# Kernel tuning notes

Hardware: AMD Instinct MI355X
Metric: run time of the kernel (lower is better)

## Reference

```python
import jax, jax.numpy as jnp
import numpy as np

DIM = 512
HEADS = 8
HEAD_DIM = DIM // HEADS


def setup_inputs() -> dict:
    key = jax.random.key(0)
    ks = jax.random.split(key, 9)
    B, T, C = 8, 8192, DIM
    s = 1.0 / np.sqrt(C)
    x = jax.random.normal(ks[0], (B, T, C), dtype=jnp.float32)
    Wq = jax.random.uniform(ks[1], (C, C), jnp.float32, -s, s)
    bq = jax.random.uniform(ks[2], (C,), jnp.float32, -s, s)
    Wk = jax.random.uniform(ks[3], (C, C), jnp.float32, -s, s)
    bk = jax.random.uniform(ks[4], (C,), jnp.float32, -s, s)
    Wv = jax.random.uniform(ks[5], (C, C), jnp.float32, -s, s)
    bv = jax.random.uniform(ks[6], (C,), jnp.float32, -s, s)
    Wo = jax.random.uniform(ks[7], (C, C), jnp.float32, -s, s)
    bo = jax.random.uniform(ks[8], (C,), jnp.float32, -s, s)
    return {"x": x, "Wq": Wq, "bq": bq, "Wk": Wk, "bk": bk,
            "Wv": Wv, "bv": bv, "Wo": Wo, "bo": bo}


def reference(x, Wq, bq, Wk, bk, Wv, bv, Wo, bo):
    B, T, C = x.shape
    H, D = HEADS, HEAD_DIM
    # projections -> [B, H, T, D]
    def proj(W, b):
        return (x @ W.T + b).reshape(B, T, H, D).transpose(0, 2, 1, 3)
    Q = proj(Wq, bq)
    K = proj(Wk, bk)
    V = proj(Wv, bv)
    # ELU+1 feature map
    Q = jax.nn.elu(Q) + 1.0
    K = jax.nn.elu(K) + 1.0
    # running KV sum (non-causal global sum) and normalizer
    KV = jnp.einsum('bhnd,bhne->bhde', K, V)          # [B,H,D,D]
    Q_KV = jnp.einsum('bhnd,bhde->bhne', Q, KV)       # [B,H,T,D]
    K_sum = K.sum(axis=2)                              # [B,H,D]
    normalizer = jnp.einsum('bhnd,bhd->bhn', Q, K_sum)  # [B,H,T]
    out = Q_KV / (normalizer[..., None] + 1e-6)
    out = out.transpose(0, 2, 1, 3).reshape(B, T, C)
    out = out @ Wo.T + bo  # dropout is identity in eval mode
    return out
```

## Files before the change

### kernel.cpp

```cpp
#include <hip/hip_runtime.h>
#include <hip/hip_bf16.h>


typedef unsigned short u16t;
typedef unsigned int   u32t;
typedef __bf16 v8bf __attribute__((ext_vector_type(8)));
typedef u16t   v8u  __attribute__((ext_vector_type(8)));
typedef float  v4f  __attribute__((ext_vector_type(4)));

static __device__ __forceinline__ float bf2f(u16t b) {
    u32t u = ((u32t)b) << 16;
    return __builtin_bit_cast(float, u);
}
static __device__ __forceinline__ u16t f2bf(float f) {
    u32t u = __builtin_bit_cast(u32t, f);
    u += 0x7fffu + ((u >> 16) & 1u);
    return (u16t)(u >> 16);
}
static __device__ __forceinline__ v8u cvt8(const float* p) {
    const float4 a = *(const float4*)p;
    const float4 b = *(const float4*)(p + 4);
    v8u r;
    r[0] = f2bf(a.x); r[1] = f2bf(a.y); r[2] = f2bf(a.z); r[3] = f2bf(a.w);
    r[4] = f2bf(b.x); r[5] = f2bf(b.y); r[6] = f2bf(b.z); r[7] = f2bf(b.w);
    return r;
}

#define GLDS16(g, l) __builtin_amdgcn_global_load_lds(                       \
        (const __attribute__((address_space(1))) void*)(g),                  \
        (__attribute__((address_space(3))) void*)(l), 16, 0, 0)

__global__ __launch_bounds__(256) void cvt_x(
        const float* __restrict__ src, u16t* __restrict__ dst) {
    const int i = (blockIdx.x * 256 + threadIdx.x) * 8;
    *(v8u*)&dst[i] = cvt8(&src[i]);
}

__global__ __launch_bounds__(256) void cvt_wb(
        const float* __restrict__ Wq, const float* __restrict__ Wk,
        const float* __restrict__ Wv, const float* __restrict__ Wo,
        const float* __restrict__ bq, const float* __restrict__ bk,
        const float* __restrict__ bv, const float* __restrict__ bo,
        u16t* __restrict__ Wpack, u16t* __restrict__ bpack) {
    const int b = blockIdx.x;
    if (b < 512) {
        const int gidx = (b * 256 + threadIdx.x) * 8;
        const int seg = gidx >> 18;
        const int off = gidx & 262143;
        const float* src = (seg == 0) ? Wq : (seg == 1) ? Wk
                          : (seg == 2) ? Wv : Wo;
        *(v8u*)&Wpack[gidx] = cvt8(&src[off]);
    } else {
        const int seg = b - 512;
        const float* src = (seg == 0) ? bq : (seg == 1) ? bk
                          : (seg == 2) ? bv : bo;
        if (threadIdx.x < 64) {
            const int off = threadIdx.x * 8;
            *(v8u*)&bpack[seg * 512 + off] = cvt8(&src[off]);
        }
    }
}

static __device__ __forceinline__ void gemm_core(
        const u16t* __restrict__ A, const u16t* __restrict__ W,
        size_t mbase, int nbase, u16t* sm, v4f acc[4][4], int tid) {
    const int w    = tid >> 6;
    const int lane = tid & 63;
    const int quad = lane >> 4;
    const int l16  = lane & 15;
    const int wm   = (w & 1) * 64;
    const int wn   = (w >> 1) * 64;

#pragma unroll
    for (int i = 0; i < 4; ++i)
#pragma unroll
        for (int j = 0; j < 4; ++j) acc[i][j] = (v4f){0.f, 0.f, 0.f, 0.f};

    const int r0 = w * 32 + (lane >> 2);
    const int r1 = r0 + 16;
    const int cs = ((lane & 3) ^ ((lane >> 3) & 3)) * 8;
    const u16t* pa0 = A + (mbase + r0) * 512 + cs;
    const u16t* pa1 = A + (mbase + r1) * 512 + cs;
    const u16t* pb0 = W + (size_t)(nbase + r0) * 512 + cs;
    const u16t* pb1 = W + (size_t)(nbase + r1) * 512 + cs;
    u16t* const la = sm + w * 1024 + lane * 8;
    u16t* const lb = sm + 8192 + w * 1024 + lane * 8;

#define GC_ISSUE(buf)                                                        \
    do {                                                                     \
        GLDS16(pa0, la + (buf) * 4096);                                      \
        GLDS16(pa1, la + (buf) * 4096 + 512);                                \
        GLDS16(pb0, lb + (buf) * 4096);                                      \
        GLDS16(pb1, lb + (buf) * 4096 + 512);                                \
        pa0 += 32; pa1 += 32; pb0 += 32; pb1 += 32;                          \
    } while (0)

    GC_ISSUE(0);
    __syncthreads();

    const int sA = (quad ^ ((l16 >> 1) & 3)) * 8;
    int cur = 0;
#pragma unroll
    for (int kt = 0; kt < 16; ++kt) {
        if (kt < 15) GC_ISSUE(cur ^ 1);
        const u16t* Ab = sm + cur * 4096;
        const u16t* Bb = sm + 8192 + cur * 4096;
        v8bf af[4], bfr[4];
#pragma unroll
        for (int mi = 0; mi < 4; ++mi)
            af[mi] = *(const v8bf*)&Ab[(wm + mi * 16 + l16) * 32 + sA];
#pragma unroll
        for (int ni = 0; ni < 4; ++ni)
            bfr[ni] = *(const v8bf*)&Bb[(wn + ni * 16 + l16) * 32 + sA];
#pragma unroll
        for (int mi = 0; mi < 4; ++mi)
#pragma unroll
            for (int ni = 0; ni < 4; ++ni)
                acc[mi][ni] = __builtin_amdgcn_mfma_f32_16x16x32_bf16(
                    af[mi], bfr[ni], acc[mi][ni], 0, 0, 0);
        __syncthreads();
        cur ^= 1;
    }
#undef GC_ISSUE
}

__global__ __launch_bounds__(256) void qkv_gemm(
        const u16t* __restrict__ xb, const u16t* __restrict__ Wpack,
        const u16t* __restrict__ bpack,
        u16t* __restrict__ Qb, u16t* __restrict__ Kb, u16t* __restrict__ Vb) {
    __shared__ __align__(16) u16t sm[16384];
    const u32t id = blockIdx.x;
    const u32t wg = (id & 7) * 768 + (id >> 3);
    const int sub = (int)(wg % 12u);
    const int p = sub >> 2;
    const int nbase = (sub & 3) * 128;
    const size_t mbase = (size_t)(wg / 12u) * 128;
    const u16t* W = Wpack + (size_t)p * 262144;
    const u16t* bias = bpack + p * 512;
    u16t* C = (p == 0) ? Qb : (p == 1) ? Kb : Vb;
    const bool elu = (p < 2);
    const int tid = threadIdx.x;
    const int w = tid >> 6, lane = tid & 63, quad = lane >> 4, l16 = lane & 15;
    const int wn = (w >> 1) * 64;

    v4f acc[4][4];
    gemm_core(xb, W, mbase, nbase, sm, acc, tid);

    u16t (*Cs)[132] = (u16t(*)[132])sm;
#pragma unroll
    for (int pass = 0; pass < 2; ++pass) {
        if ((w & 1) == pass) {
#pragma unroll
            for (int ni = 0; ni < 4; ++ni) {
                const int lcol = wn + ni * 16 + l16;
                const float bb = bf2f(bias[nbase + lcol]);
#pragma unroll
                for (int mi = 0; mi < 4; ++mi)
#pragma unroll
                    for (int r = 0; r < 4; ++r) {
                        float v = acc[mi][ni][r] + bb;
                        if (elu) v = (v > 0.f) ? (v + 1.f) : __expf(v);
                        Cs[mi * 16 + quad * 4 + r][lcol] = f2bf(v);
                    }
            }
        }
        __syncthreads();
#pragma unroll
        for (int rep = 0; rep < 4; ++rep) {
            const int f = rep * 256 + tid;
            const int row = f >> 4;
            const int c8 = (f & 15) * 8;
            const uint2 lo = *(const uint2*)&Cs[row][c8];
            const uint2 hi = *(const uint2*)&Cs[row][c8 + 4];
            const uint4 val = make_uint4(lo.x, lo.y, hi.x, hi.y);
            *(uint4*)&C[(mbase + pass * 64 + row) * 512 + nbase + c8] = val;
        }
        __syncthreads();
    }
}

__global__ __launch_bounds__(256) void out_gemm(
        const u16t* __restrict__ attn, const u16t* __restrict__ Wo,
        const u16t* __restrict__ bo, float* __restrict__ C) {
    __shared__ __align__(16) u16t sm[16384];
    const u32t id = blockIdx.x;
    const u32t wg = (id & 7) * 256 + (id >> 3);
    const int nbase = (int)(wg & 3u) * 128;
    const size_t mbase = (size_t)(wg >> 2) * 128;
    const int tid = threadIdx.x;
    const int w = tid >> 6, lane = tid & 63, quad = lane >> 4, l16 = lane & 15;
    const int wn = (w >> 1) * 64;

    v4f acc[4][4];
    gemm_core(attn, Wo, mbase, nbase, sm, acc, tid);

    float (*Cf)[132] = (float(*)[132])sm;
#pragma unroll
    for (int p = 0; p < 4; ++p) {
        if ((w & 1) == (p >> 1)) {
#pragma unroll
            for (int ni = 0; ni < 4; ++ni) {
                const int lcol = wn + ni * 16 + l16;
                const float bb = bf2f(bo[nbase + lcol]);
#pragma unroll
                for (int m2 = 0; m2 < 2; ++m2) {
                    const int mi = (p & 1) * 2 + m2;
#pragma unroll
                    for (int r = 0; r < 4; ++r)
                        Cf[m2 * 16 + quad * 4 + r][lcol] = acc[mi][ni][r] + bb;
                }
            }
        }
        __syncthreads();
#pragma unroll
        for (int rep = 0; rep < 4; ++rep) {
            const int f = rep * 256 + tid;
            const int row = f >> 5;
            const int c4 = (f & 31) * 4;
            *(float4*)&C[(mbase + p * 32 + row) * 512 + nbase + c4] =
                *(const float4*)&Cf[row][c4];
        }
        __syncthreads();
    }
}

__global__ __launch_bounds__(256) void kv_reduce(
        const u16t* __restrict__ Kp, const u16t* __restrict__ Vp,
        float* __restrict__ Part) {
    __shared__ u16t Kl[64][66];
    __shared__ u16t Vl[64][66];
    const u32t id  = blockIdx.x;
    const u32t swz = (id & 7) * 128 + (id >> 3);
    const int h     = (int)(swz & 7);
    const int grp   = (int)(swz >> 3);
    const int b     = grp >> 4;
    const int chunk = grp & 15;
    const int bh    = b * 8 + h;
    const int tid = threadIdx.x;
    const int w = tid >> 6, lane = tid & 63, quad = lane >> 4, l16 = lane & 15;
    const int trow0 = tid >> 3;
    const int c8 = (tid & 7) * 8;

    v4f acc[4];
#pragma unroll
    for (int i = 0; i < 4; ++i) acc[i] = (v4f){0.f, 0.f, 0.f, 0.f};
    float ks[8];
#pragma unroll
    for (int j = 0; j < 8; ++j) ks[j] = 0.f;

    size_t g0 = ((size_t)b * 8192 + chunk * 512 + trow0) * 512 + h * 64 + c8;
    size_t g1 = g0 + 32 * 512;
    uint4 kq0 = *(const uint4*)&Kp[g0];
    uint4 kq1 = *(const uint4*)&Kp[g1];
    uint4 vq0 = *(const uint4*)&Vp[g0];
    uint4 vq1 = *(const uint4*)&Vp[g1];

    for (int tile = 0; tile < 8; ++tile) {
        *(u32t*)&Kl[trow0][c8 + 0] = kq0.x;
        *(u32t*)&Kl[trow0][c8 + 2] = kq0.y;
        *(u32t*)&Kl[trow0][c8 + 4] = kq0.z;
        *(u32t*)&Kl[trow0][c8 + 6] = kq0.w;
        *(u32t*)&Kl[trow0 + 32][c8 + 0] = kq1.x;
        *(u32t*)&Kl[trow0 + 32][c8 + 2] = kq1.y;
        *(u32t*)&Kl[trow0 + 32][c8 + 4] = kq1.z;
        *(u32t*)&Kl[trow0 + 32][c8 + 6] = kq1.w;
        *(u32t*)&Vl[trow0][c8 + 0] = vq0.x;
        *(u32t*)&Vl[trow0][c8 + 2] = vq0.y;
        *(u32t*)&Vl[trow0][c8 + 4] = vq0.z;
        *(u32t*)&Vl[trow0][c8 + 6] = vq0.w;
        *(u32t*)&Vl[trow0 + 32][c8 + 0] = vq1.x;
        *(u32t*)&Vl[trow0 + 32][c8 + 2] = vq1.y;
        *(u32t*)&Vl[trow0 + 32][c8 + 4] = vq1.z;
        *(u32t*)&Vl[trow0 + 32][c8 + 6] = vq1.w;
        {
            const v8u ku0 = __builtin_bit_cast(v8u, kq0);
            const v8u ku1 = __builtin_bit_cast(v8u, kq1);
#pragma unroll
            for (int j = 0; j < 8; ++j)
                ks[j] += bf2f(ku0[j]) + bf2f(ku1[j]);
        }
        __syncthreads();
        if (tile < 7) {
            g0 += 64 * 512; g1 += 64 * 512;
            kq0 = *(const uint4*)&Kp[g0];
            kq1 = *(const uint4*)&Kp[g1];
            vq0 = *(const uint4*)&Vp[g0];
            vq1 = *(const uint4*)&Vp[g1];
        }
#pragma unroll
        for (int ts = 0; ts < 2; ++ts) {
            v8u au;
#pragma unroll
            for (int j = 0; j < 8; ++j)
                au[j] = Kl[ts * 32 + quad * 8 + j][w * 16 + l16];
            const v8bf af = __builtin_bit_cast(v8bf, au);
#pragma unroll
            for (int et = 0; et < 4; ++et) {
                v8u bu;
#pragma unroll
                for (int j = 0; j < 8; ++j)
                    bu[j] = Vl[ts * 32 + quad * 8 + j][et * 16 + l16];
                acc[et] = __builtin_amdgcn_mfma_f32_16x16x32_bf16(
                    af, __builtin_bit_cast(v8bf, bu), acc[et], 0, 0, 0);
            }
        }
        __syncthreads();
    }

    const size_t pbase = (size_t)(bh * 16 + chunk) * 4160;
#pragma unroll
    for (int et = 0; et < 4; ++et)
#pragma unroll
        for (int r = 0; r < 4; ++r)
            Part[pbase + (size_t)(w * 16 + quad * 4 + r) * 64 + et * 16 + l16]
                = acc[et][r];

    float* kr = (float*)&Kl[0][0];
#pragma unroll
    for (int j = 0; j < 8; ++j) kr[trow0 * 65 + c8 + j] = ks[j];
    __syncthreads();
    if (tid < 64) {
        float s = 0.f;
#pragma unroll
        for (int g = 0; g < 32; ++g) s += kr[g * 65 + tid];
        Part[pbase + 4096 + tid] = s;
    }
}

__global__ __launch_bounds__(256) void kv_pack(
        const float* __restrict__ Part, u16t* __restrict__ KVb,
        float* __restrict__ Ks) {
    __shared__ float kvs[64][64];
    const int bh = blockIdx.x;
    const int tid = threadIdx.x;
    const size_t base = (size_t)bh * 16 * 4160;
#pragma unroll
    for (int rr = 0; rr < 4; ++rr) {
        const int fi = rr * 256 + tid;
        const int d = fi >> 4;
        const int e4 = (fi & 15) * 4;
        float4 s = make_float4(0.f, 0.f, 0.f, 0.f);
        for (int c = 0; c < 16; ++c) {
            const float4 p =
                *(const float4*)&Part[base + (size_t)c * 4160 + d * 64 + e4];
            s.x += p.x; s.y += p.y; s.z += p.z; s.w += p.w;
        }
        *(float4*)&kvs[d][e4] = s;
    }
    if (tid < 64) {
        float s = 0.f;
        for (int c = 0; c < 16; ++c)
            s += Part[base + (size_t)c * 4160 + 4096 + tid];
        Ks[bh * 64 + tid] = s;
    }
    __syncthreads();
#pragma unroll
    for (int i = 0; i < 2; ++i) {
        const int c = tid + i * 256;
        const int ksi = c >> 8;
        const int nb = (c >> 6) & 3;
        const int L = c & 63;
        const int quad = L >> 4, l16 = L & 15;
        v8u pk;
#pragma unroll
        for (int j = 0; j < 8; ++j)
            pk[j] = f2bf(kvs[ksi * 32 + quad * 8 + j][nb * 16 + l16]);
        *(v8u*)&KVb[((size_t)bh * 512 + c) * 8] = pk;
    }
}

__global__ __launch_bounds__(256) void attn_apply(
        u16t* __restrict__ Q, const u16t* __restrict__ KVb,
        const float* __restrict__ Ksum) {
    __shared__ u16t Qs[128][72];
    __shared__ float ksl[64];
    __shared__ float rden[128];
    const int bx = blockIdx.x;
    const int h = blockIdx.y;
    const int b = bx >> 6;
    const int bh = b * 8 + h;
    const int tid = threadIdx.x;
    const int w = tid >> 6, lane = tid & 63, quad = lane >> 4, l16 = lane & 15;
    const size_t row0 = (size_t)bx * 128;

#pragma unroll
    for (int i = 0; i < 4; ++i) {
        const int cid = tid + i * 256;
        const int r = cid >> 3;
        const int c8 = (cid & 7) * 8;
        *(uint4*)&Qs[r][c8] = *(const uint4*)&Q[(row0 + r) * 512 + h * 64 + c8];
    }
    if (tid < 64) ksl[tid] = Ksum[bh * 64 + tid];
    __syncthreads();

    if (tid < 128) {
        float a = 1e-6f;
#pragma unroll
        for (int d = 0; d < 64; ++d) a += bf2f(Qs[tid][d]) * ksl[d];
        rden[tid] = 1.0f / fmaxf(a, 1e-9f);
    }

    v8bf bfr[2][4];
#pragma unroll
    for (int ksi = 0; ksi < 2; ++ksi)
#pragma unroll
        for (int nb = 0; nb < 4; ++nb)
            bfr[ksi][nb] = *(const v8bf*)
                &KVb[((size_t)bh * 512 + ksi * 256 + nb * 64 + lane) * 8];
    __syncthreads();

    v4f acc[2][4];
#pragma unroll
    for (int i = 0; i < 2; ++i)
#pragma unroll
        for (int j = 0; j < 4; ++j) acc[i][j] = (v4f){0.f, 0.f, 0.f, 0.f};

#pragma unroll
    for (int ksi = 0; ksi < 2; ++ksi) {
        v8bf af[2];
#pragma unroll
        for (int mt = 0; mt < 2; ++mt)
            af[mt] = *(const v8bf*)&Qs[w * 32 + mt * 16 + l16][ksi * 32 + quad * 8];
#pragma unroll
        for (int mt = 0; mt < 2; ++mt)
#pragma unroll
            for (int nb = 0; nb < 4; ++nb)
                acc[mt][nb] = __builtin_amdgcn_mfma_f32_16x16x32_bf16(
                    af[mt], bfr[ksi][nb], acc[mt][nb], 0, 0, 0);
    }

    __syncthreads();
#pragma unroll
    for (int mt = 0; mt < 2; ++mt)
#pragma unroll
        for (int nb = 0; nb < 4; ++nb)
#pragma unroll
            for (int r = 0; r < 4; ++r) {
                const int rl = w * 32 + mt * 16 + quad * 4 + r;
                const int e = nb * 16 + l16;
                Qs[rl][e] = f2bf(acc[mt][nb][r] * rden[rl]);
            }
    __syncthreads();
#pragma unroll
    for (int i = 0; i < 4; ++i) {
        const int f = i * 256 + tid;
        const int row = f >> 3;
        const int c8 = (f & 7) * 8;
        *(uint4*)&Q[(row0 + row) * 512 + h * 64 + c8] =
            *(const uint4*)&Qs[row][c8];
    }
}

extern "C" void kernel_launch(void* const* d_in, const int* in_sizes, int n_in,
                              void* d_out, int out_size, void* d_ws, size_t ws_size,
                              hipStream_t stream) {
    (void)in_sizes; (void)n_in; (void)out_size; (void)ws_size;
    const float* x32  = (const float*)d_in[0];
    const float* Wq32 = (const float*)d_in[1];
    const float* bq32 = (const float*)d_in[2];
    const float* Wk32 = (const float*)d_in[3];
    const float* bk32 = (const float*)d_in[4];
    const float* Wv32 = (const float*)d_in[5];
    const float* bv32 = (const float*)d_in[6];
    const float* Wo32 = (const float*)d_in[7];
    const float* bo32 = (const float*)d_in[8];

    u16t* xb = (u16t*)d_out;
    u16t* Vb = (u16t*)d_out + (size_t)33554432;
    float* Part = (float*)d_out;

    char* ws = (char*)d_ws;
    const size_t SZ   = (size_t)65536 * 512 * sizeof(u16t);
    const size_t KSB  = (size_t)64 * 64 * 4;
    const size_t KVbB = (size_t)64 * 512 * 16;
    u16t*  Qb    = (u16t*)(ws);
    u16t*  Kb    = (u16t*)(ws + SZ);
    float* Ks    = (float*)(ws + 2 * SZ);
    u16t*  KVb   = (u16t*)(ws + 2 * SZ + KSB);
    u16t*  Wpack = (u16t*)(ws + 2 * SZ + KSB + KVbB);
    u16t*  bpack = Wpack + (size_t)4 * 262144;

    const dim3 blk(256);
    cvt_x <<<dim3(16384), blk, 0, stream>>>(x32, xb);
    cvt_wb<<<dim3(516),   blk, 0, stream>>>(Wq32, Wk32, Wv32, Wo32,
                                            bq32, bk32, bv32, bo32,
                                            Wpack, bpack);
    qkv_gemm  <<<dim3(6144),   blk, 0, stream>>>(xb, Wpack, bpack, Qb, Kb, Vb);
    kv_reduce <<<dim3(1024),   blk, 0, stream>>>(Kb, Vb, Part);
    kv_pack   <<<dim3(64),     blk, 0, stream>>>(Part, KVb, Ks);
    attn_apply<<<dim3(512, 8), blk, 0, stream>>>(Qb, KVb, Ks);
    out_gemm  <<<dim3(2048),   blk, 0, stream>>>(Qb, Wpack + 3 * 262144,
                                                 bpack + 3 * 512,
                                                 (float*)d_out);
}
```

Before: 511.0 us.

## Triple-buffer GEMM LDS staging with explicit vmcnt waits and one barrier per step

Rewrites the shared GEMM core's K loop from a double buffer to a three-stage LDS ring. Each step issues global-to-LDS loads two tiles ahead, computes on the current tile, then waits with s_waitcnt vmcnt(4) and a raw s_barrier. Because that wait leaves the newest tile's loads outstanding, the memory latency has more time to hide behind MFMA work. In exchange each block uses 48 KB of LDS instead of 32 KB, which can lower occupancy, and a barrier is added after the core before the epilogue reuses shared memory.

```diff
diff --git a/kernel.cpp b/kernel.cpp
--- a/kernel.cpp
+++ b/kernel.cpp
@@ -29,6 +29,11 @@
 #define GLDS16(g, l) __builtin_amdgcn_global_load_lds(                       \
         (const __attribute__((address_space(1))) void*)(g),                  \
         (__attribute__((address_space(3))) void*)(l), 16, 0, 0)
+
+#define WAITV(N) asm volatile("s_waitcnt vmcnt(" #N ")" ::: "memory")
+#define BARRIER() do { __builtin_amdgcn_sched_barrier(0);                    \
+                       __builtin_amdgcn_s_barrier();                         \
+                       __builtin_amdgcn_sched_barrier(0); } while (0)
 
 __global__ __launch_bounds__(256) void cvt_x(
         const float* __restrict__ src, u16t* __restrict__ dst) {
@@ -84,43 +89,52 @@
     const u16t* pb0 = W + (size_t)(nbase + r0) * 512 + cs;
     const u16t* pb1 = W + (size_t)(nbase + r1) * 512 + cs;
     u16t* const la = sm + w * 1024 + lane * 8;
-    u16t* const lb = sm + 8192 + w * 1024 + lane * 8;
+    u16t* const lb = sm + 4096 + w * 1024 + lane * 8;
 
 #define GC_ISSUE(buf)                                                        \
     do {                                                                     \
-        GLDS16(pa0, la + (buf) * 4096);                                      \
-        GLDS16(pa1, la + (buf) * 4096 + 512);                                \
-        GLDS16(pb0, lb + (buf) * 4096);                                      \
-        GLDS16(pb1, lb + (buf) * 4096 + 512);                                \
+        GLDS16(pa0, la + (buf) * 8192);                                      \
+        GLDS16(pa1, la + (buf) * 8192 + 512);                                \
+        GLDS16(pb0, lb + (buf) * 8192);                                      \
+        GLDS16(pb1, lb + (buf) * 8192 + 512);                                \
         pa0 += 32; pa1 += 32; pb0 += 32; pb1 += 32;                          \
     } while (0)
 
-    GC_ISSUE(0);
-    __syncthreads();
-
     const int sA = (quad ^ ((l16 >> 1) & 3)) * 8;
-    int cur = 0;
-#pragma unroll
-    for (int kt = 0; kt < 16; ++kt) {
-        if (kt < 15) GC_ISSUE(cur ^ 1);
-        const u16t* Ab = sm + cur * 4096;
-        const u16t* Bb = sm + 8192 + cur * 4096;
-        v8bf af[4], bfr[4];
-#pragma unroll
-        for (int mi = 0; mi < 4; ++mi)
-            af[mi] = *(const v8bf*)&Ab[(wm + mi * 16 + l16) * 32 + sA];
-#pragma unroll
-        for (int ni = 0; ni < 4; ++ni)
-            bfr[ni] = *(const v8bf*)&Bb[(wn + ni * 16 + l16) * 32 + sA];
-#pragma unroll
-        for (int mi = 0; mi < 4; ++mi)
-#pragma unroll
-            for (int ni = 0; ni < 4; ++ni)
-                acc[mi][ni] = __builtin_amdgcn_mfma_f32_16x16x32_bf16(
-                    af[mi], bfr[ni], acc[mi][ni], 0, 0, 0);
-        __syncthreads();
-        cur ^= 1;
-    }
+
+#define GC_COMPUTE(RB)                                                       \
+    do {                                                                     \
+        const u16t* Ab_ = sm + (RB) * 8192;                                  \
+        const u16t* Bb_ = Ab_ + 4096;                                        \
+        v8bf af_[4], bf_[4];                                                 \
+        _Pragma("unroll")                                                    \
+        for (int mi = 0; mi < 4; ++mi)                                       \
+            af_[mi] = *(const v8bf*)&Ab_[(wm + mi * 16 + l16) * 32 + sA];    \
+        _Pragma("unroll")                                                    \
+        for (int ni = 0; ni < 4; ++ni)                                       \
+            bf_[ni] = *(const v8bf*)&Bb_[(wn + ni * 16 + l16) * 32 + sA];    \
+        _Pragma("unroll")                                                    \
+        for (int mi = 0; mi < 4; ++mi)                                       \
+            _Pragma("unroll")                                                \
+            for (int ni = 0; ni < 4; ++ni)                                   \
+                acc[mi][ni] = __builtin_amdgcn_mfma_f32_16x16x32_bf16(       \
+                    af_[mi], bf_[ni], acc[mi][ni], 0, 0, 0);                 \
+    } while (0)
+
+#define GC_STEP(RB, IB)                                                      \
+    do { GC_ISSUE(IB); GC_COMPUTE(RB); WAITV(4); BARRIER(); } while (0)
+
+    GC_ISSUE(0); GC_ISSUE(1);
+    WAITV(4); BARRIER();
+    GC_STEP(0, 2); GC_STEP(1, 0); GC_STEP(2, 1);
+    GC_STEP(0, 2); GC_STEP(1, 0); GC_STEP(2, 1);
+    GC_STEP(0, 2); GC_STEP(1, 0); GC_STEP(2, 1);
+    GC_STEP(0, 2); GC_STEP(1, 0); GC_STEP(2, 1);
+    GC_STEP(0, 2); GC_STEP(1, 0);
+    GC_COMPUTE(2); WAITV(0); BARRIER();
+    GC_COMPUTE(0);
+#undef GC_STEP
+#undef GC_COMPUTE
 #undef GC_ISSUE
 }
 
@@ -128,7 +142,7 @@
         const u16t* __restrict__ xb, const u16t* __restrict__ Wpack,
         const u16t* __restrict__ bpack,
         u16t* __restrict__ Qb, u16t* __restrict__ Kb, u16t* __restrict__ Vb) {
-    __shared__ __align__(16) u16t sm[16384];
+    __shared__ __align__(16) u16t sm[24576];
     const u32t id = blockIdx.x;
     const u32t wg = (id & 7) * 768 + (id >> 3);
     const int sub = (int)(wg % 12u);
@@ -145,6 +159,7 @@
 
     v4f acc[4][4];
     gemm_core(xb, W, mbase, nbase, sm, acc, tid);
+    __syncthreads();
 
     u16t (*Cs)[132] = (u16t(*)[132])sm;
 #pragma unroll
@@ -182,7 +197,7 @@
 __global__ __launch_bounds__(256) void out_gemm(
         const u16t* __restrict__ attn, const u16t* __restrict__ Wo,
         const u16t* __restrict__ bo, float* __restrict__ C) {
-    __shared__ __align__(16) u16t sm[16384];
+    __shared__ __align__(16) u16t sm[24576];
     const u32t id = blockIdx.x;
     const u32t wg = (id & 7) * 256 + (id >> 3);
     const int nbase = (int)(wg & 3u) * 128;
@@ -193,6 +208,7 @@
 
     v4f acc[4][4];
     gemm_core(attn, Wo, mbase, nbase, sm, acc, tid);
+    __syncthreads();
 
     float (*Cf)[132] = (float(*)[132])sm;
 #pragma unroll
```

Measured after the change: 494.3 us. 3.3% less time.

## Use 256x256 GEMM tiles with 4-stage LDS pipeline and 8 warps

Applied to the files above, without the earlier changes.

Replaces the 128x128, 4-warp, double-buffered GEMM core with a 256x256 tile per 512-thread block. It uses a 4-deep global_load_lds ring buffer with explicit vmcnt/lgkmcnt waits, sched barriers and setprio around the MFMA bursts. The larger tile raises arithmetic intensity and cuts redundant global loads of x and W, while the deeper pipeline hides load latency. In exchange it uses 128KB of LDS per block and more accumulator registers, which may limit occupancy, and it launches fewer blocks.

```diff
diff --git a/kernel.cpp b/kernel.cpp
--- a/kernel.cpp
+++ b/kernel.cpp
@@ -29,6 +29,13 @@
 #define GLDS16(g, l) __builtin_amdgcn_global_load_lds(                       \
         (const __attribute__((address_space(1))) void*)(g),                  \
         (__attribute__((address_space(3))) void*)(l), 16, 0, 0)
+
+#define WAITV(N) asm volatile("s_waitcnt vmcnt(" #N ")" ::: "memory")
+#define BARRIER() do { __builtin_amdgcn_sched_barrier(0);                    \
+                       __builtin_amdgcn_s_barrier();                         \
+                       __builtin_amdgcn_sched_barrier(0); } while (0)
+#define LGKM0() do { asm volatile("s_waitcnt lgkmcnt(0)" ::: "memory");      \
+                     __builtin_amdgcn_sched_barrier(0); } while (0)
 
 __global__ __launch_bounds__(256) void cvt_x(
         const float* __restrict__ src, u16t* __restrict__ dst) {
@@ -61,101 +68,122 @@
     }
 }
 
-static __device__ __forceinline__ void gemm_core(
+static __device__ __forceinline__ void gemm256_core(
         const u16t* __restrict__ A, const u16t* __restrict__ W,
-        size_t mbase, int nbase, u16t* sm, v4f acc[4][4], int tid) {
-    const int w    = tid >> 6;
-    const int lane = tid & 63;
-    const int quad = lane >> 4;
-    const int l16  = lane & 15;
-    const int wm   = (w & 1) * 64;
-    const int wn   = (w >> 1) * 64;
-
-#pragma unroll
-    for (int i = 0; i < 4; ++i)
+        size_t mbase, int nbase, u16t* sm, v4f acc[8][4], int tid) {
+    const int lane = tid & 63, w = tid >> 6;
+    const int quad = lane >> 4, l16 = lane & 15;
+    const int wr = w >> 2, wc = w & 3;
+
+#pragma unroll
+    for (int i = 0; i < 8; ++i)
 #pragma unroll
         for (int j = 0; j < 4; ++j) acc[i][j] = (v4f){0.f, 0.f, 0.f, 0.f};
 
-    const int r0 = w * 32 + (lane >> 2);
-    const int r1 = r0 + 16;
-    const int cs = ((lane & 3) ^ ((lane >> 3) & 3)) * 8;
-    const u16t* pa0 = A + (mbase + r0) * 512 + cs;
-    const u16t* pa1 = A + (mbase + r1) * 512 + cs;
-    const u16t* pb0 = W + (size_t)(nbase + r0) * 512 + cs;
-    const u16t* pb1 = W + (size_t)(nbase + r1) * 512 + cs;
-    u16t* const la = sm + w * 1024 + lane * 8;
-    u16t* const lb = sm + 8192 + w * 1024 + lane * 8;
-
-#define GC_ISSUE(buf)                                                        \
-    do {                                                                     \
-        GLDS16(pa0, la + (buf) * 4096);                                      \
-        GLDS16(pa1, la + (buf) * 4096 + 512);                                \
-        GLDS16(pb0, lb + (buf) * 4096);                                      \
-        GLDS16(pb1, lb + (buf) * 4096 + 512);                                \
-        pa0 += 32; pa1 += 32; pb0 += 32; pb1 += 32;                          \
+    const int rS   = (tid >> 2) & 63;
+    const int wrqS = tid >> 8;
+    const u16t* pa = A + (mbase + wrqS * 128 + rS) * 512
+                       + ((tid & 3) ^ (rS & 3)) * 8;
+    const int rB = tid >> 2;
+    const u16t* pb = W + (size_t)(nbase + rB) * 512
+                       + ((tid & 3) ^ (rB & 3)) * 8;
+    u16t* const dA = sm + tid * 8;
+    u16t* const dB = sm + 8192 + tid * 8;
+
+    const int sl8 = (quad ^ (l16 & 3)) * 8;
+    const int aRd = wr * 2048 + l16 * 32 + sl8;
+    const int bRd = 8192 + (wc * 64 + l16) * 32 + sl8;
+
+#define ST_A(sb, kt) do {                                                    \
+        GLDS16(pa + (kt) * 32, dA + (sb) * 16384);                           \
+        GLDS16(pa + 64 * 512 + (kt) * 32, dA + (sb) * 16384 + 4096);         \
     } while (0)
-
-    GC_ISSUE(0);
-    __syncthreads();
-
-    const int sA = (quad ^ ((l16 >> 1) & 3)) * 8;
-    int cur = 0;
-#pragma unroll
-    for (int kt = 0; kt < 16; ++kt) {
-        if (kt < 15) GC_ISSUE(cur ^ 1);
-        const u16t* Ab = sm + cur * 4096;
-        const u16t* Bb = sm + 8192 + cur * 4096;
-        v8bf af[4], bfr[4];
-#pragma unroll
-        for (int mi = 0; mi < 4; ++mi)
-            af[mi] = *(const v8bf*)&Ab[(wm + mi * 16 + l16) * 32 + sA];
-#pragma unroll
-        for (int ni = 0; ni < 4; ++ni)
-            bfr[ni] = *(const v8bf*)&Bb[(wn + ni * 16 + l16) * 32 + sA];
-#pragma unroll
-        for (int mi = 0; mi < 4; ++mi)
-#pragma unroll
-            for (int ni = 0; ni < 4; ++ni)
-                acc[mi][ni] = __builtin_amdgcn_mfma_f32_16x16x32_bf16(
-                    af[mi], bfr[ni], acc[mi][ni], 0, 0, 0);
-        __syncthreads();
-        cur ^= 1;
-    }
-#undef GC_ISSUE
-}
-
-__global__ __launch_bounds__(256) void qkv_gemm(
+#define ST_B(sb, kt) do {                                                    \
+        GLDS16(pb + (kt) * 32, dB + (sb) * 16384);                           \
+        GLDS16(pb + 128 * 512 + (kt) * 32, dB + (sb) * 16384 + 4096);        \
+    } while (0)
+
+    ST_A(0, 0); ST_B(0, 0); ST_A(1, 1); ST_B(1, 1);
+    WAITV(4); BARRIER();
+
+#pragma unroll
+    for (int t = 0; t < 16; ++t) {
+        const int buf = (t & 3) * 16384;
+        const int sb  = (t + 2) & 3;
+        v8bf af[4], bf[4];
+#pragma unroll
+        for (int j = 0; j < 4; ++j)
+            af[j] = *(const v8bf*)&sm[buf + aRd + j * 512];
+#pragma unroll
+        for (int n = 0; n < 4; ++n)
+            bf[n] = *(const v8bf*)&sm[buf + bRd + n * 512];
+        if (t < 14) ST_A(sb, t + 2);
+        BARRIER();
+        LGKM0();
+        __builtin_amdgcn_s_setprio(1);
+#pragma unroll
+        for (int j = 0; j < 4; ++j)
+#pragma unroll
+            for (int n = 0; n < 4; ++n)
+                acc[j][n] = __builtin_amdgcn_mfma_f32_16x16x32_bf16(
+                    af[j], bf[n], acc[j][n], 0, 0, 0);
+        __builtin_amdgcn_s_setprio(0);
+        BARRIER();
+#pragma unroll
+        for (int j = 0; j < 4; ++j)
+            af[j] = *(const v8bf*)&sm[buf + 4096 + aRd + j * 512];
+        if (t < 14) ST_B(sb, t + 2);
+        BARRIER();
+        LGKM0();
+        __builtin_amdgcn_s_setprio(1);
+#pragma unroll
+        for (int j = 0; j < 4; ++j)
+#pragma unroll
+            for (int n = 0; n < 4; ++n)
+                acc[4 + j][n] = __builtin_amdgcn_mfma_f32_16x16x32_bf16(
+                    af[j], bf[n], acc[4 + j][n], 0, 0, 0);
+        __builtin_amdgcn_s_setprio(0);
+        if (t <= 13)      { WAITV(4); }
+        else if (t == 14) { WAITV(0); }
+        BARRIER();
+    }
+#undef ST_A
+#undef ST_B
+}
+
+__global__ __launch_bounds__(512, 2) void qkv_gemm(
         const u16t* __restrict__ xb, const u16t* __restrict__ Wpack,
         const u16t* __restrict__ bpack,
         u16t* __restrict__ Qb, u16t* __restrict__ Kb, u16t* __restrict__ Vb) {
-    __shared__ __align__(16) u16t sm[16384];
+    __shared__ __align__(16) u16t sm[65536];
     const u32t id = blockIdx.x;
-    const u32t wg = (id & 7) * 768 + (id >> 3);
-    const int sub = (int)(wg % 12u);
-    const int p = sub >> 2;
-    const int nbase = (sub & 3) * 128;
-    const size_t mbase = (size_t)(wg / 12u) * 128;
-    const u16t* W = Wpack + (size_t)p * 262144;
+    const u32t wg = (id & 7) * 192 + (id >> 3);
+    const int sub = (int)(wg % 6u);
+    const int p = sub >> 1;
+    const int nbase = (sub & 1) * 256;
+    const size_t mbase = (size_t)(wg / 6u) * 256;
+    const u16t* Wt = Wpack + (size_t)p * 262144;
     const u16t* bias = bpack + p * 512;
     u16t* C = (p == 0) ? Qb : (p == 1) ? Kb : Vb;
     const bool elu = (p < 2);
     const int tid = threadIdx.x;
     const int w = tid >> 6, lane = tid & 63, quad = lane >> 4, l16 = lane & 15;
-    const int wn = (w >> 1) * 64;
-
-    v4f acc[4][4];
-    gemm_core(xb, W, mbase, nbase, sm, acc, tid);
-
-    u16t (*Cs)[132] = (u16t(*)[132])sm;
+    const int wr = w >> 2, wc = w & 3;
+
+    v4f acc[8][4];
+    gemm256_core(xb, Wt, mbase, nbase, sm, acc, tid);
+    __syncthreads();
+
+    u16t (*Cs)[264] = (u16t(*)[264])sm;
 #pragma unroll
     for (int pass = 0; pass < 2; ++pass) {
-        if ((w & 1) == pass) {
+        if (wr == pass) {
 #pragma unroll
             for (int ni = 0; ni < 4; ++ni) {
-                const int lcol = wn + ni * 16 + l16;
+                const int lcol = wc * 64 + ni * 16 + l16;
                 const float bb = bf2f(bias[nbase + lcol]);
 #pragma unroll
-                for (int mi = 0; mi < 4; ++mi)
+                for (int mi = 0; mi < 8; ++mi)
 #pragma unroll
                     for (int r = 0; r < 4; ++r) {
                         float v = acc[mi][ni][r] + bb;
@@ -166,59 +194,58 @@
         }
         __syncthreads();
 #pragma unroll
-        for (int rep = 0; rep < 4; ++rep) {
-            const int f = rep * 256 + tid;
-            const int row = f >> 4;
-            const int c8 = (f & 15) * 8;
-            const uint2 lo = *(const uint2*)&Cs[row][c8];
-            const uint2 hi = *(const uint2*)&Cs[row][c8 + 4];
-            const uint4 val = make_uint4(lo.x, lo.y, hi.x, hi.y);
-            *(uint4*)&C[(mbase + pass * 64 + row) * 512 + nbase + c8] = val;
+        for (int rd = 0; rd < 8; ++rd) {
+            const int f = rd * 512 + tid;
+            const int row = f >> 5;
+            const int sl = f & 31;
+            *(uint4*)&C[(mbase + pass * 128 + row) * 512 + nbase + sl * 8] =
+                *(const uint4*)&Cs[row][sl * 8];
         }
         __syncthreads();
     }
 }
 
-__global__ __launch_bounds__(256) void out_gemm(
+__global__ __launch_bounds__(512, 2) void out_gemm(
         const u16t* __restrict__ attn, const u16t* __restrict__ Wo,
         const u16t* __restrict__ bo, float* __restrict__ C) {
-    __shared__ __align__(16) u16t sm[16384];
+    __shared__ __align__(16) u16t sm[65536];
     const u32t id = blockIdx.x;
-    const u32t wg = (id & 7) * 256 + (id >> 3);
-    const int nbase = (int)(wg & 3u) * 128;
-    const size_t mbase = (size_t)(wg >> 2) * 128;
+    const u32t wg = (id & 7) * 64 + (id >> 3);
+    const int nbase = (int)(wg & 1u) * 256;
+    const size_t mbase = (size_t)(wg >> 1) * 256;
     const int tid = threadIdx.x;
     const int w = tid >> 6, lane = tid & 63, quad = lane >> 4, l16 = lane & 15;
-    const int wn = (w >> 1) * 64;
-
-    v4f acc[4][4];
-    gemm_core(attn, Wo, mbase, nbase, sm, acc, tid);
-
-    float (*Cf)[132] = (float(*)[132])sm;
-#pragma unroll
-    for (int p = 0; p < 4; ++p) {
-        if ((w & 1) == (p >> 1)) {
+    const int wr = w >> 2, wc = w & 3;
+
+    v4f acc[8][4];
+    gemm256_core(attn, Wo, mbase, nbase, sm, acc, tid);
+    __syncthreads();
+
+    float (*Cf)[264] = (float(*)[264])sm;
+#pragma unroll
+    for (int pass = 0; pass < 4; ++pass) {
+        if (wr == (pass >> 1)) {
 #pragma unroll
             for (int ni = 0; ni < 4; ++ni) {
-                const int lcol = wn + ni * 16 + l16;
+                const int lcol = wc * 64 + ni * 16 + l16;
                 const float bb = bf2f(bo[nbase + lcol]);
 #pragma unroll
-                for (int m2 = 0; m2 < 2; ++m2) {
-                    const int mi = (p & 1) * 2 + m2;
+                for (int j = 0; j < 4; ++j) {
+                    const int mi = (pass & 1) * 4 + j;
 #pragma unroll
                     for (int r = 0; r < 4; ++r)
-                        Cf[m2 * 16 + quad * 4 + r][lcol] = acc[mi][ni][r] + bb;
+                        Cf[j * 16 + quad * 4 + r][lcol] = acc[mi][ni][r] + bb;
                 }
             }
         }
         __syncthreads();
 #pragma unroll
-        for (int rep = 0; rep < 4; ++rep) {
-            const int f = rep * 256 + tid;
-            const int row = f >> 5;
-            const int c4 = (f & 31) * 4;
-            *(float4*)&C[(mbase + p * 32 + row) * 512 + nbase + c4] =
-                *(const float4*)&Cf[row][c4];
+        for (int rd = 0; rd < 8; ++rd) {
+            const int f = rd * 512 + tid;
+            const int row = f >> 6;
+            const int sl = f & 63;
+            *(float4*)&C[(mbase + pass * 64 + row) * 512 + nbase + sl * 4] =
+                *(const float4*)&Cf[row][sl * 4];
         }
         __syncthreads();
     }
@@ -485,11 +512,12 @@
     cvt_wb<<<dim3(516),   blk, 0, stream>>>(Wq32, Wk32, Wv32, Wo32,
                                             bq32, bk32, bv32, bo32,
                                             Wpack, bpack);
-    qkv_gemm  <<<dim3(6144),   blk, 0, stream>>>(xb, Wpack, bpack, Qb, Kb, Vb);
+    qkv_gemm  <<<dim3(1536), dim3(512), 0, stream>>>(xb, Wpack, bpack,
+                                                     Qb, Kb, Vb);
     kv_reduce <<<dim3(1024),   blk, 0, stream>>>(Kb, Vb, Part);
     kv_pack   <<<dim3(64),     blk, 0, stream>>>(Part, KVb, Ks);
     attn_apply<<<dim3(512, 8), blk, 0, stream>>>(Qb, KVb, Ks);
-    out_gemm  <<<dim3(2048),   blk, 0, stream>>>(Qb, Wpack + 3 * 262144,
-                                                 bpack + 3 * 512,
-                                                 (float*)d_out);
-}
+    out_gemm  <<<dim3(512), dim3(512), 0, stream>>>(Qb, Wpack + 3 * 262144,
+                                                    bpack + 3 * 512,
+                                                    (float*)d_out);
+}
```

Result: no change. 503.0 us (-1.6%).
